# Performance work log

Hardware: AMD Instinct MI355X
Metric: run time of the kernel (lower is better)

The kernel has to match this reference:

```python
import jax, jax.numpy as jnp
import numpy as np

B, S, DIM = 2, 4096, 1024
H, HD = 16, 64          # num_heads, head_dim (DIM = H*HD)
KN = 64                 # k neighbors per query
SCALE = 1.0 / np.sqrt(HD)
CANTOR_DEPTH = 8


def _cantor_coords(seq_len: int, depth: int = CANTOR_DEPTH) -> np.ndarray:
    """Vectorized replica of CantorAttention._compute_cantor_coord."""
    x = np.arange(seq_len, dtype=np.float64) / max(1, seq_len - 1)
    x = np.clip(x, 1e-06, 1.0 - 1e-06)
    val = np.zeros(seq_len, dtype=np.float64)
    factor = 0.5
    for _ in range(depth):
        xs = x * 3.0
        digit = np.floor(xs)
        x = xs - digit
        val += factor * (digit == 2)
        factor *= 0.5
    return val.astype(np.float32)


def _build_routes(seq_len: int, k: int) -> np.ndarray:
    coords = _cantor_coords(seq_len)
    dist = np.abs(coords[:, None] - coords[None, :])  # [S, S]
    routes = np.argsort(dist, axis=1, kind='stable')[:, :k]  # k smallest
    return routes.astype(np.int32)


def setup_inputs() -> dict:
    key = jax.random.key(0)
    kx, kw1, kb1, kw2, kb2 = jax.random.split(key, 5)
    x = jax.random.normal(kx, (B, S, DIM), dtype=jnp.float32)
    # learned params (qkv and out projections)
    W_qkv = jax.random.normal(kw1, (DIM, 3 * DIM), dtype=jnp.float32) * (1.0 / np.sqrt(DIM))
    b_qkv = jax.random.normal(kb1, (3 * DIM,), dtype=jnp.float32) * 0.01
    W_out = jax.random.normal(kw2, (DIM, DIM), dtype=jnp.float32) * (1.0 / np.sqrt(DIM))
    b_out = jax.random.normal(kb2, (DIM,), dtype=jnp.float32) * 0.01
    routes = jnp.asarray(_build_routes(S, KN))  # [S, KN] int32, positional Cantor kNN
    return {"x": x, "W_qkv": W_qkv, "b_qkv": b_qkv, "W_out": W_out, "b_out": b_out, "routes": routes}


def reference(x, W_qkv, b_qkv, W_out, b_out, routes):
    Bs, Sl, _ = x.shape
    qkv = x @ W_qkv + b_qkv                                   # [B,S,3*DIM]
    qkv = qkv.reshape(Bs, Sl, 3, H, HD).transpose(2, 0, 3, 1, 4)
    q, k, v = qkv[0], qkv[1], qkv[2]                          # [B,H,S,HD]
    k_g = k[:, :, routes, :]                                  # [B,H,S,KN,HD]
    v_g = v[:, :, routes, :]                                  # [B,H,S,KN,HD]
    scores = jnp.einsum('bhqd,bhqkd->bhqk', q, k_g) * SCALE   # [B,H,S,KN]
    attn = jax.nn.softmax(scores, axis=-1)
    out = jnp.einsum('bhqk,bhqkd->bhqd', attn, v_g)           # [B,H,S,HD]
    out = out.transpose(0, 2, 1, 3).reshape(Bs, Sl, DIM)
    return out @ W_out + b_out
```

## Files before the change

### kernel.cpp

```cpp
#include <hip/hip_runtime.h>
#include <hip/hip_bf16.h>
#include <stdint.h>

#define DEVI __device__ __forceinline__

typedef __bf16 bf16x8 __attribute__((ext_vector_type(8)));
typedef float f32x4 __attribute__((ext_vector_type(4)));
typedef unsigned short ushort8v __attribute__((ext_vector_type(8)));

static constexpr int SEQ = 4096;
static constexpr int DIM_ = 1024;
static constexpr int NH = 16;
static constexpr int HD_ = 64;
static constexpr float SCALE_ = 0.125f;

DEVI unsigned short f2bf(float f) {
  __hip_bfloat16 h = __float2bfloat16(f);
  return __builtin_bit_cast(unsigned short, h);
}


__global__ void k_cvt_bf16(const float* __restrict__ in, unsigned short* __restrict__ out) {
  int i = (blockIdx.x * 256 + threadIdx.x) * 4;
  float4 v = *reinterpret_cast<const float4*>(in + i);
  ushort4 o;
  o.x = f2bf(v.x); o.y = f2bf(v.y); o.z = f2bf(v.z); o.w = f2bf(v.w);
  *reinterpret_cast<ushort4*>(out + i) = o;
}

__global__ void k_transpose_cvt(const float* __restrict__ in, unsigned short* __restrict__ out,
                                int K, int N) {
  __shared__ float tile[64][65];
  const int n0 = blockIdx.x * 64, k0 = blockIdx.y * 64;
  const int tr = threadIdx.x >> 6, tc = threadIdx.x & 63;
#pragma unroll
  for (int p = 0; p < 16; ++p) {
    int r = p * 4 + tr;
    tile[r][tc] = in[(size_t)(k0 + r) * N + n0 + tc];
  }
  __syncthreads();
#pragma unroll
  for (int p = 0; p < 16; ++p) {
    int r = p * 4 + tr;
    out[(size_t)(n0 + r) * K + k0 + tc] = f2bf(tile[tc][r]);
  }
}


DEVI void load16_lds(const void* g, void* l) {
  __builtin_amdgcn_global_load_lds((__attribute__((address_space(1))) void*)(g),
                                   (__attribute__((address_space(3))) void*)(l),
                                   16, 0, 0);
}

template <int MODE>
__global__ __launch_bounds__(256, 4)
void k_gemm_bt(const unsigned short* __restrict__ A,
               const unsigned short* __restrict__ Bt,
               const float* __restrict__ bias,
               float* __restrict__ outF,
               unsigned short* __restrict__ outQ,
               unsigned short* __restrict__ outK,
               unsigned short* __restrict__ outV,
               int M, int N, int K) {
  constexpr int BK = 32;
  __shared__ alignas(16) unsigned short As[2][128 * BK];
  __shared__ alignas(16) unsigned short Bs[2][128 * BK];
  const int tid = threadIdx.x;
  const int wave = tid >> 6, lane = tid & 63;
  const int wr = wave >> 1, wc = wave & 1;
  const int l15 = lane & 15, q = lane >> 4;
  const int bm = blockIdx.x * 128, bn = blockIdx.y * 128;

  f32x4 acc[4][4] = {};

  const int srow = lane >> 2;
  const int scol = ((lane & 3) ^ ((lane >> 3) & 3)) * 8;
  const unsigned short* aS0 = A + (size_t)(bm + wave * 16 + srow) * K + scol;
  const unsigned short* aS1 = aS0 + (size_t)64 * K;
  const unsigned short* bS0 = Bt + (size_t)(bn + wave * 16 + srow) * K + scol;
  const unsigned short* bS1 = bS0 + (size_t)64 * K;
  const int dOff = (wave * 16) * BK;

  const int x3 = (l15 >> 1) & 3;
  const int aRdOff = (wr * 64 + l15) * BK + (q ^ x3) * 8;
  const int bRdOff = (wc * 64 + l15) * BK + (q ^ x3) * 8;

  load16_lds(aS0, &As[0][dOff]);
  load16_lds(aS1, &As[0][dOff + 64 * BK]);
  load16_lds(bS0, &Bs[0][dOff]);
  load16_lds(bS1, &Bs[0][dOff + 64 * BK]);
  __syncthreads();

  const int NT = K / BK;
#pragma unroll 1
  for (int t = 0; t < NT; ++t) {
    const int cur = t & 1;
    if (t + 1 < NT) {
      const int k1 = (t + 1) * BK;
      const int nxt = cur ^ 1;
      load16_lds(aS0 + k1, &As[nxt][dOff]);
      load16_lds(aS1 + k1, &As[nxt][dOff + 64 * BK]);
      load16_lds(bS0 + k1, &Bs[nxt][dOff]);
      load16_lds(bS1 + k1, &Bs[nxt][dOff + 64 * BK]);
    }

    bf16x8 af[4], bfr[4];
#pragma unroll
    for (int m = 0; m < 4; ++m)
      af[m] = *reinterpret_cast<const bf16x8*>(&As[cur][aRdOff + m * 16 * BK]);
#pragma unroll
    for (int n = 0; n < 4; ++n)
      bfr[n] = *reinterpret_cast<const bf16x8*>(&Bs[cur][bRdOff + n * 16 * BK]);
#pragma unroll
    for (int m = 0; m < 4; ++m)
#pragma unroll
      for (int n = 0; n < 4; ++n)
        acc[m][n] = __builtin_amdgcn_mfma_f32_16x16x32_bf16(af[m], bfr[n], acc[m][n], 0, 0, 0);

    __syncthreads();
  }

  const int r0 = q * 4;
#pragma unroll
  for (int m = 0; m < 4; ++m) {
#pragma unroll
    for (int n = 0; n < 4; ++n) {
      const int col = bn + wc * 64 + n * 16 + l15;
      const float bv = bias[col];
#pragma unroll
      for (int j = 0; j < 4; ++j) {
        const int row = bm + wr * 64 + m * 16 + r0 + j;
        const float v = acc[m][n][j] + bv;
        if constexpr (MODE == 0) {
          outF[(size_t)row * N + col] = v;
        } else {
          const int t = col >> 10;
          const int hh = (col >> 6) & 15;
          const int d = col & 63;
          const int b = row >> 12;
          const int s = row & 4095;
          unsigned short* dst = (t == 0) ? outQ : (t == 1) ? outK : outV;
          dst[((size_t)(b * NH + hh) * SEQ + s) * HD_ + d] = f2bf(v);
        }
      }
    }
  }
}


__global__ void k_init(int* __restrict__ tileQ, int* __restrict__ cnt,
                       int* __restrict__ pos, int* __restrict__ nTiles) {
  const int i = blockIdx.x * 256 + threadIdx.x;
  tileQ[i] = -1;
  if (i < 4096) { cnt[i] = 0; pos[i] = 0; }
  if (i == 0) *nTiles = 0;
}

__global__ void k_gid(const int* __restrict__ routes, int* __restrict__ gid, int* __restrict__ cnt) {
  const int s = blockIdx.x * 256 + threadIdx.x;
  const int lead = routes[s * 64];
  int g = s;
  if (lead >= 0 && lead < SEQ && lead != s) {
    bool eq = true;
    const int4* a = reinterpret_cast<const int4*>(routes + (size_t)s * 64);
    const int4* b = reinterpret_cast<const int4*>(routes + (size_t)lead * 64);
#pragma unroll
    for (int i = 0; i < 16; ++i) {
      int4 x = a[i], y = b[i];
      eq = eq && (x.x == y.x) && (x.y == y.y) && (x.z == y.z) && (x.w == y.w);
    }
    if (eq) g = lead;
  }
  gid[s] = g;
  atomicAdd(&cnt[g], 1);
}

__global__ void k_tilebase(const int* __restrict__ cnt, int* __restrict__ tileBase,
                           int* __restrict__ nTiles) {
  const int g = blockIdx.x * 256 + threadIdx.x;
  const int c = cnt[g];
  if (c > 0) {
    tileBase[g] = atomicAdd(nTiles, (c + 15) >> 4);
  }
}

__global__ void k_scatter(const int* __restrict__ gid, const int* __restrict__ tileBase,
                          int* __restrict__ pos, int* __restrict__ tileQ,
                          int* __restrict__ tileLead) {
  const int s = blockIdx.x * 256 + threadIdx.x;
  const int g = gid[s];
  const int p = atomicAdd(&pos[g], 1);
  const int tile = tileBase[g] + (p >> 4);
  tileQ[tile * 16 + (p & 15)] = s;
  if ((p & 15) == 0) tileLead[tile] = g;
}


__global__ __launch_bounds__(256, 3)
void k_attn_grp(const unsigned short* __restrict__ Q,
                const unsigned short* __restrict__ Kb,
                const unsigned short* __restrict__ Vb,
                const int* __restrict__ routes,
                const int* __restrict__ tileQ,
                const int* __restrict__ tileLead,
                const int* __restrict__ nTilesPtr,
                unsigned short* __restrict__ att) {
  const int nT = *nTilesPtr;

  __shared__ int sMemRaw[16];
  __shared__ int sMemEff[16];
  __shared__ int sRoutes[64];
  __shared__ alignas(16) unsigned short sV[4][4096];
  __shared__ alignas(16) unsigned short sP[4][16 * 72];

  const int tid = threadIdx.x;
  const int wave = tid >> 6, lane = tid & 63;
  unsigned short* VL = sV[wave];
  unsigned short* P = sP[wave];
  const int hi = lane >> 4;
  const int l15 = lane & 15;
  const int l7 = lane & 7;
  const int rr = lane >> 3;

  const int bh = blockIdx.x * 4 + wave;
  const size_t base = (size_t)bh * (SEQ * HD_);
  const int b = bh >> 4, h = bh & 15;

  for (int tile = blockIdx.y; tile < nT; tile += gridDim.y) {
    __syncthreads();
    if (tid < 16) {
      const int v = tileQ[tile * 16 + tid];
      const int v0 = tileQ[tile * 16];
      sMemRaw[tid] = v;
      sMemEff[tid] = (v < 0) ? v0 : v;
    } else if (tid >= 64 && tid < 128) {
      const int lead = tileLead[tile];
      sRoutes[tid - 64] = routes[(size_t)lead * 64 + (tid - 64)];
    }
    __syncthreads();

    bf16x8 qa0, qa1;
    {
      const unsigned short* qrow = Q + base + (size_t)sMemEff[l15] * HD_ + hi * 8;
      qa0 = *reinterpret_cast<const bf16x8*>(qrow);
      qa1 = *reinterpret_cast<const bf16x8*>(qrow + 32);
    }

    bf16x8 kf0[4], kf1[4];
#pragma unroll
    for (int nb = 0; nb < 4; ++nb) {
      const int rk = sRoutes[nb * 16 + l15];
      const unsigned short* krow = Kb + base + (size_t)rk * HD_ + hi * 8;
      kf0[nb] = *reinterpret_cast<const bf16x8*>(krow);
      kf1[nb] = *reinterpret_cast<const bf16x8*>(krow + 32);
    }

    {
#pragma unroll
      for (int t = 0; t < 8; ++t) {
        const int rk = sRoutes[t * 8 + rr];
        const int sc = ((l7 - 2 * (t & 3)) & 7) * 8;
        load16_lds(Vb + base + (size_t)rk * HD_ + sc, &VL[t * 512]);
      }
    }

    asm volatile("s_waitcnt vmcnt(8)" ::: "memory");
    __builtin_amdgcn_sched_barrier(0);

    f32x4 accS[4] = {};
    __builtin_amdgcn_s_setprio(1);
#pragma unroll
    for (int nb = 0; nb < 4; ++nb) {
      accS[nb] = __builtin_amdgcn_mfma_f32_16x16x32_bf16(qa0, kf0[nb], accS[nb], 0, 0, 0);
      accS[nb] = __builtin_amdgcn_mfma_f32_16x16x32_bf16(qa1, kf1[nb], accS[nb], 0, 0, 0);
    }
    __builtin_amdgcn_s_setprio(0);

#pragma unroll
    for (int jj = 0; jj < 4; ++jj) {
      float m = fmaxf(fmaxf(accS[0][jj], accS[1][jj]), fmaxf(accS[2][jj], accS[3][jj]));
#pragma unroll
      for (int o = 1; o < 16; o <<= 1) m = fmaxf(m, __shfl_xor(m, o));
      const float e0 = __expf((accS[0][jj] - m) * SCALE_);
      const float e1 = __expf((accS[1][jj] - m) * SCALE_);
      const float e2 = __expf((accS[2][jj] - m) * SCALE_);
      const float e3 = __expf((accS[3][jj] - m) * SCALE_);
      float sum = (e0 + e1) + (e2 + e3);
#pragma unroll
      for (int o = 1; o < 16; o <<= 1) sum += __shfl_xor(sum, o);
      const float rs = __builtin_amdgcn_rcpf(sum);
      const int row = hi * 4 + jj;
      P[row * 72 + 0 + l15] = f2bf(e0 * rs);
      P[row * 72 + 16 + l15] = f2bf(e1 * rs);
      P[row * 72 + 32 + l15] = f2bf(e2 * rs);
      P[row * 72 + 48 + l15] = f2bf(e3 * rs);
    }

    asm volatile("s_waitcnt vmcnt(0) lgkmcnt(0)" ::: "memory");
    __builtin_amdgcn_sched_barrier(0);

    f32x4 accO[4] = {};
#pragma unroll
    for (int ks = 0; ks < 2; ++ks) {
      bf16x8 pf = *reinterpret_cast<const bf16x8*>(&P[l15 * 72 + ks * 32 + hi * 8]);
#pragma unroll
      for (int nb = 0; nb < 4; ++nb) {
        const int d = nb * 16 + l15;
        const int rot = (d + 16 * hi) & 63;
        bf16x8 vf;
#pragma unroll
        for (int j = 0; j < 8; ++j) {
          const int k = ks * 32 + hi * 8 + j;
          vf[j] = *reinterpret_cast<const __bf16*>(&VL[k * 64 + rot]);
        }
        __builtin_amdgcn_s_setprio(1);
        accO[nb] = __builtin_amdgcn_mfma_f32_16x16x32_bf16(pf, vf, accO[nb], 0, 0, 0);
        __builtin_amdgcn_s_setprio(0);
      }
    }

#pragma unroll
    for (int jj = 0; jj < 4; ++jj) {
      const int sQ = sMemRaw[hi * 4 + jj];
      if (sQ >= 0) {
#pragma unroll
        for (int nb = 0; nb < 4; ++nb) {
          att[((size_t)(b * SEQ + sQ)) * DIM_ + h * HD_ + nb * 16 + l15] = f2bf(accO[nb][jj]);
        }
      }
    }
  }
}


extern "C" void kernel_launch(void* const* d_in, const int* in_sizes, int n_in,
                              void* d_out, int out_size, void* d_ws, size_t ws_size,
                              hipStream_t stream) {
  (void)in_sizes; (void)n_in; (void)out_size; (void)ws_size;
  const float* x      = (const float*)d_in[0];
  const float* Wqkv   = (const float*)d_in[1];
  const float* bqkv   = (const float*)d_in[2];
  const float* Wout   = (const float*)d_in[3];
  const float* bout   = (const float*)d_in[4];
  const int*   routes = (const int*)d_in[5];
  float* out = (float*)d_out;

  uint8_t* ws = (uint8_t*)d_ws;
  unsigned short* wqkvT = (unsigned short*)(ws);
  unsigned short* woutT = (unsigned short*)(ws + 6291456);
  unsigned short* Qb    = (unsigned short*)(ws + 8388608);
  unsigned short* Kb    = (unsigned short*)(ws + 25165824);
  unsigned short* Vb    = (unsigned short*)(ws + 41943040);
  unsigned short* att   = (unsigned short*)(ws + 58720256);

  unsigned short* xb = (unsigned short*)d_out;
  uint8_t* g0 = (uint8_t*)d_out + (16u << 20);
  int* gidArr   = (int*)(g0);
  int* cnt      = (int*)(g0 + 16384);
  int* pos      = (int*)(g0 + 32768);
  int* tileBase = (int*)(g0 + 49152);
  int* nTiles   = (int*)(g0 + 65536);
  int* tileLead = (int*)(g0 + 81920);
  int* tileQ    = (int*)(g0 + 98304);

  k_init<<<256, 256, 0, stream>>>(tileQ, cnt, pos, nTiles);
  k_gid<<<16, 256, 0, stream>>>(routes, gidArr, cnt);
  k_tilebase<<<16, 256, 0, stream>>>(cnt, tileBase, nTiles);
  k_scatter<<<16, 256, 0, stream>>>(gidArr, tileBase, pos, tileQ, tileLead);

  k_cvt_bf16<<<8192, 256, 0, stream>>>(x, xb);
  k_transpose_cvt<<<dim3(48, 16), 256, 0, stream>>>(Wqkv, wqkvT, 1024, 3072);
  k_transpose_cvt<<<dim3(16, 16), 256, 0, stream>>>(Wout, woutT, 1024, 1024);

  k_gemm_bt<1><<<dim3(64, 24), 256, 0, stream>>>(xb, wqkvT, bqkv, nullptr, Qb, Kb, Vb,
                                                 8192, 3072, 1024);
  k_attn_grp<<<dim3(8, 96), 256, 0, stream>>>(Qb, Kb, Vb, routes, tileQ, tileLead,
                                              nTiles, att);
  k_gemm_bt<0><<<dim3(64, 8), 256, 0, stream>>>(att, woutT, bout, out,
                                                nullptr, nullptr, nullptr, 8192, 1024, 1024);
}
```

Before: 154.7 us.

## Transpose V through registers into swizzled LDS for vectorized PV fragment reads

Replaces the async global-to-LDS row copy of gathered V with per-lane register loads of whole V rows, then writes them transposed into LDS with an XOR swizzle. The PV MFMA B operand can then be read as one 16-byte LDS load per fragment instead of eight scalar 2-byte reads. The cost is 64 scalar LDS stores per lane and a full vmcnt(0) wait right after the QK MFMAs, which exposes V gather latency before the softmax instead of overlapping it.

New measurement: 163.0 us. +5.3%, slower.

```diff
diff --git a/kernel.cpp b/kernel.cpp
--- a/kernel.cpp
+++ b/kernel.cpp
@@ -211,17 +211,15 @@
   __shared__ int sMemRaw[16];
   __shared__ int sMemEff[16];
   __shared__ int sRoutes[64];
-  __shared__ alignas(16) unsigned short sV[4][4096];
+  __shared__ alignas(16) unsigned short sVt[4][4096];
   __shared__ alignas(16) unsigned short sP[4][16 * 72];
 
   const int tid = threadIdx.x;
   const int wave = tid >> 6, lane = tid & 63;
-  unsigned short* VL = sV[wave];
+  unsigned short* VT = sVt[wave];
   unsigned short* P = sP[wave];
   const int hi = lane >> 4;
   const int l15 = lane & 15;
-  const int l7 = lane & 7;
-  const int rr = lane >> 3;
 
   const int bh = blockIdx.x * 4 + wave;
   const size_t base = (size_t)bh * (SEQ * HD_);
@@ -256,13 +254,13 @@
       kf1[nb] = *reinterpret_cast<const bf16x8*>(krow + 32);
     }
 
+    ushort8v vreg[8];
     {
-#pragma unroll
-      for (int t = 0; t < 8; ++t) {
-        const int rk = sRoutes[t * 8 + rr];
-        const int sc = ((l7 - 2 * (t & 3)) & 7) * 8;
-        load16_lds(Vb + base + (size_t)rk * HD_ + sc, &VL[t * 512]);
-      }
+      const int rkv = sRoutes[lane];
+      const unsigned short* vrow = Vb + base + (size_t)rkv * HD_;
+#pragma unroll
+      for (int c = 0; c < 8; ++c)
+        vreg[c] = *reinterpret_cast<const ushort8v*>(vrow + c * 8);
     }
 
     asm volatile("s_waitcnt vmcnt(8)" ::: "memory");
@@ -276,6 +274,20 @@
       accS[nb] = __builtin_amdgcn_mfma_f32_16x16x32_bf16(qa1, kf1[nb], accS[nb], 0, 0, 0);
     }
     __builtin_amdgcn_s_setprio(0);
+
+    asm volatile("s_waitcnt vmcnt(0)" ::: "memory");
+    __builtin_amdgcn_sched_barrier(0);
+    {
+      const int khi = lane >> 3, klo = lane & 7;
+#pragma unroll
+      for (int c = 0; c < 8; ++c) {
+#pragma unroll
+        for (int j = 0; j < 8; ++j) {
+          const int d = c * 8 + j;
+          VT[d * 64 + ((khi ^ (d & 7)) << 3) + klo] = (unsigned short)vreg[c][j];
+        }
+      }
+    }
 
 #pragma unroll
     for (int jj = 0; jj < 4; ++jj) {
@@ -297,7 +309,7 @@
       P[row * 72 + 48 + l15] = f2bf(e3 * rs);
     }
 
-    asm volatile("s_waitcnt vmcnt(0) lgkmcnt(0)" ::: "memory");
+    asm volatile("s_waitcnt lgkmcnt(0)" ::: "memory");
     __builtin_amdgcn_sched_barrier(0);
 
     f32x4 accO[4] = {};
@@ -307,13 +319,8 @@
 #pragma unroll
       for (int nb = 0; nb < 4; ++nb) {
         const int d = nb * 16 + l15;
-        const int rot = (d + 16 * hi) & 63;
-        bf16x8 vf;
-#pragma unroll
-        for (int j = 0; j < 8; ++j) {
-          const int k = ks * 32 + hi * 8 + j;
-          vf[j] = *reinterpret_cast<const __bf16*>(&VL[k * 64 + rot]);
-        }
+        bf16x8 vf = *reinterpret_cast<const bf16x8*>(
+            &VT[d * 64 + (((ks * 4 + hi) ^ (d & 7)) << 3)]);
         __builtin_amdgcn_s_setprio(1);
         accO[nb] = __builtin_amdgcn_mfma_f32_16x16x32_bf16(pf, vf, accO[nb], 0, 0, 0);
         __builtin_amdgcn_s_setprio(0);
```
